# Kernel optimization log

Measured on AMD Instinct MI355X. Metric: run time of the kernel, lower is better.

## Reference

```python
import jax, jax.numpy as jnp
import numpy as np

N_NODES = 50000
N_FEAT = 128
N_EDGES = 1600000
HID = 64


def gcn_conv(x, row, col, w, W, b, n):
    """PyG GCNConv with edge weights and added self-loops (fill_value=1).
    x: [N, Fin]; row/col: [E] (src, dst); w: [E]; W: [Fin, Fout]; b: [Fout].
    """
    loop = jnp.arange(n)
    r = jnp.concatenate([row, loop])
    c = jnp.concatenate([col, loop])
    ww = jnp.concatenate([w, jnp.ones((n,), dtype=x.dtype)])
    deg = jax.ops.segment_sum(ww, c, num_segments=n)  # [N]
    dinv = jnp.where(deg > 0, jax.lax.rsqrt(deg), 0.0)
    norm = dinv[r] * ww * dinv[c]  # [E+N]
    xw = x @ W  # [N, Fout] -- linear before propagate, as in PyG
    msg = norm[:, None] * xw[r]  # gather + scale
    out = jax.ops.segment_sum(msg, c, num_segments=n)  # scatter-add
    return out + b


def setup_inputs() -> dict:
    key = jax.random.key(0)
    ks = jax.random.split(key, 12)
    features = jax.random.normal(ks[0], (N_NODES, N_FEAT), dtype=jnp.float32)
    edge_index = jax.random.randint(ks[1], (2, N_EDGES), 0, N_NODES, dtype=jnp.int64)
    edge_attr = jax.random.uniform(ks[2], (N_EDGES,), dtype=jnp.float32)
    s = 0.05
    # generator encoder: GCNConv(n_feat->64), GCNConv(64->n_feat)
    Wg1 = jax.random.normal(ks[3], (N_FEAT, HID), dtype=jnp.float32) * s
    bg1 = jnp.zeros((HID,), dtype=jnp.float32)
    Wg2 = jax.random.normal(ks[4], (HID, N_FEAT), dtype=jnp.float32) * s
    bg2 = jnp.zeros((N_FEAT,), dtype=jnp.float32)
    # discriminator: GCNConv(n_feat->64), Linear(n_nodes*64 -> 1)
    Wd1 = jax.random.normal(ks[5], (N_FEAT, HID), dtype=jnp.float32) * s
    bd1 = jnp.zeros((HID,), dtype=jnp.float32)
    wfc = jax.random.normal(ks[6], (N_NODES * HID,), dtype=jnp.float32) * 0.001
    bfc = jnp.zeros((), dtype=jnp.float32)
    return {"features": features, "edge_index": edge_index, "edge_attr": edge_attr,
            "Wg1": Wg1, "bg1": bg1, "Wg2": Wg2, "bg2": bg2,
            "Wd1": Wd1, "bd1": bd1, "wfc": wfc, "bfc": bfc}


def reference(features, edge_index, edge_attr, Wg1, bg1, Wg2, bg2, Wd1, bd1, wfc, bfc):
    n = features.shape[0]
    row, col = edge_index[0], edge_index[1]
    # --- generator encoder (eval mode: dropout is a no-op) ---
    h = gcn_conv(features, row, col, edge_attr, Wg1, bg1, n)
    h = jax.nn.relu(h)
    z = jax.nn.sigmoid(gcn_conv(h, row, col, edge_attr, Wg2, bg2, n))  # [N, n_feat]
    # --- GAE inner-product decoder over the given edge list ---
    edge_probs = jax.nn.sigmoid(jnp.sum(z[row] * z[col], axis=-1))  # [E]
    # residual connection
    enc = z + features
    edge_probs = jnp.nan_to_num(edge_probs, nan=0.0)
    # --- discriminator (eval mode: no noise, no dropout) ---
    d = gcn_conv(enc, row, col, edge_probs, Wd1, bd1, n)
    d = jax.nn.relu(d)
    logit = jnp.dot(d.reshape(-1), wfc) + bfc
    return jax.nn.sigmoid(logit)
```

## Files before the change

### kernel.cpp

```cpp
#include <hip/hip_runtime.h>
#include <math.h>

static constexpr int NN = 50000;
static constexpr int NF = 128;
static constexpr int NH = 64;
static constexpr int NE = 1600000;
static constexpr int NBUSED = (NN + 255) / 256;
static constexpr int NWG = 256;
static constexpr int CHUNK = NE / NWG;

typedef unsigned long long u64;


__device__ __forceinline__ float bf2f(unsigned u) { return __uint_as_float(u << 16); }
__device__ __forceinline__ unsigned short f2bf(float f) {
  unsigned b = __float_as_uint(f);
  b += 0x7fffu + ((b >> 16) & 1u);
  return (unsigned short)(b >> 16);
}
__device__ __forceinline__ float sigm(float x) { return 1.f / (1.f + __expf(-x)); }


__global__ __launch_bounds__(256) void bhist_k(const int* __restrict__ col,
                                               int* __restrict__ counts) {
  __shared__ int cnt[256];
  cnt[threadIdx.x] = 0;
  __syncthreads();
  int g = blockIdx.x;
  int e1 = g * CHUNK + CHUNK;
  for (int e = g * CHUNK + threadIdx.x; e < e1; e += 256)
    atomicAdd(&cnt[col[e] >> 8], 1);
  __syncthreads();
  counts[g * 256 + threadIdx.x] = cnt[threadIdx.x];
}

__global__ __launch_bounds__(256) void bscan_k(int* __restrict__ counts) {
  __shared__ int sm[256];
  int b = threadIdx.x;
  int tot = 0;
  for (int g = 0; g < NWG; g++) tot += counts[g * 256 + b];
  sm[b] = tot;
  __syncthreads();
  int v = tot;
  for (int off = 1; off < 256; off <<= 1) {
    int u = (b >= off) ? sm[b - off] : 0;
    __syncthreads();
    sm[b] += u;
    __syncthreads();
  }
  int run = sm[b] - v;
  for (int g = 0; g < NWG; g++) {
    int c = counts[g * 256 + b];
    counts[g * 256 + b] = run;
    run += c;
  }
}

__global__ __launch_bounds__(256) void bpart_k(const int* __restrict__ row,
                                               const int* __restrict__ col,
                                               const float* __restrict__ w,
                                               const int* __restrict__ counts,
                                               u64* __restrict__ ebuf) {
  __shared__ int cur[256];
  int g = blockIdx.x;
  cur[threadIdx.x] = counts[g * 256 + threadIdx.x];
  __syncthreads();
  int e1 = g * CHUNK + CHUNK;
  for (int e = g * CHUNK + threadIdx.x; e < e1; e += 256) {
    int c = col[e];
    int p = atomicAdd(&cur[c >> 8], 1);
    u64 pk = ((u64)(unsigned)__float_as_int(w[e]) << 32) |
             ((unsigned)(c & 255) << 16) | (unsigned)row[e];
    ebuf[p] = pk;
  }
}

__global__ __launch_bounds__(256) void bsortA_k(const u64* __restrict__ ebuf,
                                                const int* __restrict__ counts,
                                                int* __restrict__ rowstart,
                                                float* __restrict__ dinv) {
  __shared__ int cnt[256];
  __shared__ float deg[256];
  __shared__ int sm[256];
  int b = blockIdx.x, t = threadIdx.x;
  cnt[t] = 0;
  deg[t] = 1.0f;
  __syncthreads();
  int boff = counts[b];
  int bend = (b < NBUSED - 1) ? counts[b + 1] : NE;
  for (int e = boff + t; e < bend; e += 256) {
    u64 pk = ebuf[e];
    unsigned lo = (unsigned)pk;
    int c = (lo >> 16) & 255;
    atomicAdd(&cnt[c], 1);
    atomicAdd(&deg[c], __uint_as_float((unsigned)(pk >> 32)));
  }
  __syncthreads();
  int v = cnt[t];
  sm[t] = v;
  __syncthreads();
  for (int off = 1; off < 256; off <<= 1) {
    int u = (t >= off) ? sm[t - off] : 0;
    __syncthreads();
    sm[t] += u;
    __syncthreads();
  }
  int colg = b * 256 + t;
  if (colg < NN) {
    rowstart[colg] = boff + sm[t] - v;
    dinv[colg] = rsqrtf(deg[t]);
  }
  if (b == NBUSED - 1 && t == 0) rowstart[NN] = NE;
}

__global__ __launch_bounds__(256) void bsortB_k(const u64* __restrict__ ebuf,
                                                const int* __restrict__ counts,
                                                const int* __restrict__ rowstart,
                                                const float* __restrict__ dinv,
                                                int2* __restrict__ es) {
  __shared__ int cur[256];
  int b = blockIdx.x, t = threadIdx.x;
  int colg = b * 256 + t;
  cur[t] = (colg < NN) ? rowstart[colg] : NE;
  __syncthreads();
  int boff = counts[b];
  int bend = (b < NBUSED - 1) ? counts[b + 1] : NE;
  for (int e = boff + t; e < bend; e += 256) {
    u64 pk = ebuf[e];
    unsigned lo = (unsigned)pk;
    int r = lo & 0xffff;
    int c = (lo >> 16) & 255;
    float wv = __uint_as_float((unsigned)(pk >> 32));
    int p = atomicAdd(&cur[c], 1);
    es[p] = make_int2(r, __float_as_int(dinv[r] * wv));
  }
}

__global__ void norm2_k(int2* __restrict__ es, const float* __restrict__ ep_s,
                        const float* __restrict__ dinv2, int E) {
  int e = blockIdx.x * 256 + threadIdx.x;
  if (e < E) {
    int2 v = es[e];
    es[e] = make_int2(v.x, __float_as_int(dinv2[v.x] * ep_s[e]));
  }
}

template<int K, int M, int ACT, bool OUTF, bool OUTH, bool XH>
__global__ __launch_bounds__(256) void gemm_k(const float* __restrict__ X,
                                              const unsigned short* __restrict__ Xh,
                                              const float* __restrict__ Xadd,
                                              const float* __restrict__ W,
                                              const float* __restrict__ bias,
                                              float* __restrict__ Yf,
                                              unsigned short* __restrict__ Yh) {
  __shared__ float Ws[K * M];
  __shared__ float Xs[16][K];
  for (int i = threadIdx.x; i < K * M; i += 256) Ws[i] = W[i];
  int r0 = blockIdx.x * 16;
  for (int i = threadIdx.x; i < 16 * K; i += 256) {
    int r = i / K, k = i % K;
    size_t off = (size_t)(r0 + r) * K + k;
    float v = XH ? bf2f(Xh[off]) : X[off];
    if (Xadd) v += Xadd[off];
    Xs[r][k] = v;
  }
  __syncthreads();
  constexpr int RPT = 16 * M / 256;
  constexpr int RS = 256 / M;
  int colc = threadIdx.x % M;
  int rb = threadIdx.x / M;
  float acc[RPT];
#pragma unroll
  for (int i = 0; i < RPT; i++) acc[i] = 0.f;
  for (int k = 0; k < K; k++) {
    float wv = Ws[k * M + colc];
#pragma unroll
    for (int i = 0; i < RPT; i++) acc[i] += Xs[rb + i * RS][k] * wv;
  }
#pragma unroll
  for (int i = 0; i < RPT; i++) {
    int r = r0 + rb + i * RS;
    float o = acc[i];
    if (ACT > 0) o += bias[colc];
    if (ACT == 2) o = sigm(o);
    if (OUTF) Yf[(size_t)r * M + colc] = o;
    if (OUTH) Yh[(size_t)r * M + colc] = f2bf(o);
  }
}

template<int MODE>
__global__ __launch_bounds__(256) void agg64_k(const int* __restrict__ rowstart,
                                               const int2* __restrict__ es,
                                               const unsigned short* __restrict__ src,
                                               const float* __restrict__ dinv,
                                               const float* __restrict__ bias,
                                               unsigned short* __restrict__ outh,
                                               float* __restrict__ outf,
                                               const float* __restrict__ wfc) {
  int wid = (blockIdx.x * 256 + threadIdx.x) >> 6;
  int lane = threadIdx.x & 63;
  int sub = lane >> 4;
  int l = lane & 15;
  int e0 = rowstart[wid], e1 = rowstart[wid + 1];
  float a0 = 0.f, a1 = 0.f, a2 = 0.f, a3 = 0.f;
  for (int eb = e0; eb < e1; eb += 4) {
    int e = eb + sub;
    bool valid = e < e1;
    int2 er = es[valid ? e : eb];
    float nm = valid ? __int_as_float(er.y) : 0.f;
    ushort4 v = *(const ushort4*)(src + (size_t)er.x * 64 + l * 4);
    a0 = fmaf(nm, bf2f(v.x), a0);
    a1 = fmaf(nm, bf2f(v.y), a1);
    a2 = fmaf(nm, bf2f(v.z), a2);
    a3 = fmaf(nm, bf2f(v.w), a3);
  }
  a0 += __shfl_xor(a0, 16); a0 += __shfl_xor(a0, 32);
  a1 += __shfl_xor(a1, 16); a1 += __shfl_xor(a1, 32);
  a2 += __shfl_xor(a2, 16); a2 += __shfl_xor(a2, 32);
  a3 += __shfl_xor(a3, 16); a3 += __shfl_xor(a3, 32);
  float di = dinv[wid];
  ushort4 sv = *(const ushort4*)(src + (size_t)wid * 64 + l * 4);
  float o0 = di * (a0 + di * bf2f(sv.x));
  float o1 = di * (a1 + di * bf2f(sv.y));
  float o2 = di * (a2 + di * bf2f(sv.z));
  float o3 = di * (a3 + di * bf2f(sv.w));
  if (MODE != 1) {
    float4 b = *(const float4*)(bias + l * 4);
    o0 = fmaxf(o0 + b.x, 0.f);
    o1 = fmaxf(o1 + b.y, 0.f);
    o2 = fmaxf(o2 + b.z, 0.f);
    o3 = fmaxf(o3 + b.w, 0.f);
  }
  if (MODE == 0) {
    if (sub == 0) {
      ushort4 p;
      p.x = f2bf(o0); p.y = f2bf(o1); p.z = f2bf(o2); p.w = f2bf(o3);
      *(ushort4*)(outh + (size_t)wid * 64 + l * 4) = p;
    }
  } else if (MODE == 1) {
    if (sub == 0) *(float4*)(outf + (size_t)wid * 64 + l * 4) = make_float4(o0, o1, o2, o3);
  } else {
    float s = 0.f;
    if (sub == 0) {
      float4 w4 = *(const float4*)(wfc + (size_t)wid * 64 + l * 4);
      s = o0 * w4.x + o1 * w4.y + o2 * w4.z + o3 * w4.w;
    }
    s += __shfl_xor(s, 1);
    s += __shfl_xor(s, 2);
    s += __shfl_xor(s, 4);
    s += __shfl_xor(s, 8);
    __shared__ float bs[4];
    if (lane == 0) bs[threadIdx.x >> 6] = s;
    __syncthreads();
    if (threadIdx.x == 0) outf[blockIdx.x] = bs[0] + bs[1] + bs[2] + bs[3];
  }
}

__global__ __launch_bounds__(256) void eprob8_k(const int* __restrict__ rowstart,
                                                const int2* __restrict__ es,
                                                const unsigned short* __restrict__ zh,
                                                float* __restrict__ ep_s,
                                                float* __restrict__ dinv2) {
  int wid = (blockIdx.x * 256 + threadIdx.x) >> 6;
  int lane = threadIdx.x & 63;
  int sub = lane >> 3;
  int l = lane & 7;
  const unsigned short* zp = zh + (size_t)wid * NF + l * 16;
  uint4 zA = *(const uint4*)zp;
  uint4 zB = *(const uint4*)(zp + 8);
  float z0 = bf2f(zA.x & 0xffffu), z1 = bf2f(zA.x >> 16);
  float z2 = bf2f(zA.y & 0xffffu), z3 = bf2f(zA.y >> 16);
  float z4 = bf2f(zA.z & 0xffffu), z5 = bf2f(zA.z >> 16);
  float z6 = bf2f(zA.w & 0xffffu), z7 = bf2f(zA.w >> 16);
  float z8 = bf2f(zB.x & 0xffffu), z9 = bf2f(zB.x >> 16);
  float za = bf2f(zB.y & 0xffffu), zb = bf2f(zB.y >> 16);
  float zc = bf2f(zB.z & 0xffffu), zd = bf2f(zB.z >> 16);
  float ze = bf2f(zB.w & 0xffffu), zf = bf2f(zB.w >> 16);
  int e0 = rowstart[wid], e1 = rowstart[wid + 1];
  float sum = 0.f;
  for (int eb = e0; eb < e1; eb += 8) {
    int e = eb + sub;
    bool valid = e < e1;
    int r = es[valid ? e : eb].x;
    const unsigned short* rp = zh + (size_t)r * NF + l * 16;
    uint4 a = *(const uint4*)rp;
    uint4 b = *(const uint4*)(rp + 8);
    float d;
    d  = bf2f(a.x & 0xffffu) * z0 + bf2f(a.x >> 16) * z1;
    d += bf2f(a.y & 0xffffu) * z2 + bf2f(a.y >> 16) * z3;
    d += bf2f(a.z & 0xffffu) * z4 + bf2f(a.z >> 16) * z5;
    d += bf2f(a.w & 0xffffu) * z6 + bf2f(a.w >> 16) * z7;
    d += bf2f(b.x & 0xffffu) * z8 + bf2f(b.x >> 16) * z9;
    d += bf2f(b.y & 0xffffu) * za + bf2f(b.y >> 16) * zb;
    d += bf2f(b.z & 0xffffu) * zc + bf2f(b.z >> 16) * zd;
    d += bf2f(b.w & 0xffffu) * ze + bf2f(b.w >> 16) * zf;
    d += __shfl_xor(d, 1);
    d += __shfl_xor(d, 2);
    d += __shfl_xor(d, 4);
    if (valid && l == 0) {
      float p = sigm(d);
      ep_s[e] = p;
      sum += p;
    }
  }
  sum += __shfl_xor(sum, 8);
  sum += __shfl_xor(sum, 16);
  sum += __shfl_xor(sum, 32);
  if (lane == 0) dinv2[wid] = rsqrtf(1.f + sum);
}

__global__ __launch_bounds__(256) void reduce_k(const float* __restrict__ partials, int n,
                                                const float* __restrict__ bfc,
                                                float* __restrict__ out) {
  float s = 0.f;
  for (int i = threadIdx.x; i < n; i += 256) s += partials[i];
  s += __shfl_xor(s, 1);
  s += __shfl_xor(s, 2);
  s += __shfl_xor(s, 4);
  s += __shfl_xor(s, 8);
  s += __shfl_xor(s, 16);
  s += __shfl_xor(s, 32);
  __shared__ float ws4[4];
  if ((threadIdx.x & 63) == 0) ws4[threadIdx.x >> 6] = s;
  __syncthreads();
  if (threadIdx.x == 0) out[0] = sigm(ws4[0] + ws4[1] + ws4[2] + ws4[3] + bfc[0]);
}


extern "C" void kernel_launch(void* const* d_in, const int* in_sizes, int n_in,
                              void* d_out, int out_size, void* d_ws, size_t ws_size,
                              hipStream_t stream) {
  const float* features = (const float*)d_in[0];
  const int* edge_index = (const int*)d_in[1];
  const float* edge_attr = (const float*)d_in[2];
  const float* Wg1 = (const float*)d_in[3];
  const float* bg1 = (const float*)d_in[4];
  const float* Wg2 = (const float*)d_in[5];
  const float* bg2 = (const float*)d_in[6];
  const float* Wd1 = (const float*)d_in[7];
  const float* bd1 = (const float*)d_in[8];
  const float* wfc = (const float*)d_in[9];
  const float* bfc = (const float*)d_in[10];
  float* out = (float*)d_out;

  const int* row = edge_index;
  const int* col = edge_index + NE;

  char* wsb = (char*)d_ws;
  auto carve = [&](size_t bytes) {
    void* p = wsb;
    wsb += (bytes + 255) & ~(size_t)255;
    return p;
  };
  int*   counts   = (int*)carve((size_t)NWG * 256 * 4);
  int*   rowstart = (int*)carve((NN + 1) * 4);
  float* dinv     = (float*)carve(NN * 4);
  float* dinv2    = (float*)carve(NN * 4);
  u64*   ebuf     = (u64*)carve((size_t)NE * 8);
  int2*  es       = (int2*)carve((size_t)NE * 8);
  float* ep_s     = (float*)carve((size_t)NE * 4);
  unsigned short* xwh = (unsigned short*)carve((size_t)NN * NH * 2);
  unsigned short* hh  = (unsigned short*)carve((size_t)NN * NH * 2);
  float* ah   = (float*)carve((size_t)NN * NH * 4);
  unsigned short* zh = (unsigned short*)carve((size_t)NN * NF * 2);
  float* partials = (float*)carve(12500 * 4);

  const int GE = (NE + 255) / 256;
  const int GG = NN / 16;
  const int GW = NN * 64 / 256;

  bhist_k<<<NWG, 256, 0, stream>>>(col, counts);
  bscan_k<<<1, 256, 0, stream>>>(counts);
  bpart_k<<<NWG, 256, 0, stream>>>(row, col, edge_attr, counts, ebuf);
  bsortA_k<<<NBUSED, 256, 0, stream>>>(ebuf, counts, rowstart, dinv);
  bsortB_k<<<NBUSED, 256, 0, stream>>>(ebuf, counts, rowstart, dinv, es);

  gemm_k<NF, NH, 0, false, true, false><<<GG, 256, 0, stream>>>(
      features, nullptr, nullptr, Wg1, nullptr, nullptr, xwh);
  agg64_k<0><<<GW, 256, 0, stream>>>(rowstart, es, xwh, dinv, bg1, hh, nullptr, nullptr);

  agg64_k<1><<<GW, 256, 0, stream>>>(rowstart, es, hh, dinv, nullptr, nullptr, ah, nullptr);
  gemm_k<NH, NF, 2, false, true, false><<<GG, 256, 0, stream>>>(
      ah, nullptr, nullptr, Wg2, bg2, nullptr, zh);

  eprob8_k<<<GW, 256, 0, stream>>>(rowstart, es, zh, ep_s, dinv2);

  norm2_k<<<GE, 256, 0, stream>>>(es, ep_s, dinv2, NE);

  gemm_k<NF, NH, 0, false, true, true><<<GG, 256, 0, stream>>>(
      nullptr, zh, features, Wd1, nullptr, nullptr, xwh);
  agg64_k<2><<<GW, 256, 0, stream>>>(rowstart, es, xwh, dinv2, bd1, nullptr, partials, wfc);

  reduce_k<<<1, 256, 0, stream>>>(partials, GW, bfc, out);
}
```

Baseline: 401.0 us.

## Gather FP8 z and discriminator features, fold norm2 into aggregation

Stores z and the discriminator's x@W as FP8 (e4m3 via the hardware cvt builtins) so the edge-probability and final aggregation gathers move half the bytes of the earlier bf16 copies. The separate norm2 pass is removed: eprob writes the edge probability straight into the edge-list slot, and the final aggregation applies dinv2[src] on the fly. The bf16 aggregations now use 16-byte loads with 8 edges per wavefront iteration. The cost is a large drop in precision for z and xw, which risks accuracy tolerance, plus an extra dinv2 gather per edge.

```diff
diff --git a/kernel.cpp b/kernel.cpp
--- a/kernel.cpp
+++ b/kernel.cpp
@@ -10,6 +10,7 @@
 static constexpr int CHUNK = NE / NWG;
 
 typedef unsigned long long u64;
+typedef float f32x2 __attribute__((ext_vector_type(2)));
 
 
 __device__ __forceinline__ float bf2f(unsigned u) { return __uint_as_float(u << 16); }
@@ -19,6 +20,21 @@
   return (unsigned short)(b >> 16);
 }
 __device__ __forceinline__ float sigm(float x) { return 1.f / (1.f + __expf(-x)); }
+__device__ __forceinline__ unsigned char f2fp8(float f) {
+  int v = __builtin_amdgcn_cvt_pk_fp8_f32(f, f, 0, false);
+  return (unsigned char)(v & 0xff);
+}
+__device__ __forceinline__ void fp8x16_dec(uint4 v, float* o) {
+  f32x2 t;
+  t = __builtin_amdgcn_cvt_pk_f32_fp8(v.x, false); o[0] = t.x;  o[1] = t.y;
+  t = __builtin_amdgcn_cvt_pk_f32_fp8(v.x, true);  o[2] = t.x;  o[3] = t.y;
+  t = __builtin_amdgcn_cvt_pk_f32_fp8(v.y, false); o[4] = t.x;  o[5] = t.y;
+  t = __builtin_amdgcn_cvt_pk_f32_fp8(v.y, true);  o[6] = t.x;  o[7] = t.y;
+  t = __builtin_amdgcn_cvt_pk_f32_fp8(v.z, false); o[8] = t.x;  o[9] = t.y;
+  t = __builtin_amdgcn_cvt_pk_f32_fp8(v.z, true);  o[10] = t.x; o[11] = t.y;
+  t = __builtin_amdgcn_cvt_pk_f32_fp8(v.w, false); o[12] = t.x; o[13] = t.y;
+  t = __builtin_amdgcn_cvt_pk_f32_fp8(v.w, true);  o[14] = t.x; o[15] = t.y;
+}
 
 
 __global__ __launch_bounds__(256) void bhist_k(const int* __restrict__ col,
@@ -136,23 +152,15 @@
   }
 }
 
-__global__ void norm2_k(int2* __restrict__ es, const float* __restrict__ ep_s,
-                        const float* __restrict__ dinv2, int E) {
-  int e = blockIdx.x * 256 + threadIdx.x;
-  if (e < E) {
-    int2 v = es[e];
-    es[e] = make_int2(v.x, __float_as_int(dinv2[v.x] * ep_s[e]));
-  }
-}
-
-template<int K, int M, int ACT, bool OUTF, bool OUTH, bool XH>
+template<int K, int M, int ACT, bool OUTF, bool OUTH, bool XH, bool OUT8>
 __global__ __launch_bounds__(256) void gemm_k(const float* __restrict__ X,
                                               const unsigned short* __restrict__ Xh,
                                               const float* __restrict__ Xadd,
                                               const float* __restrict__ W,
                                               const float* __restrict__ bias,
                                               float* __restrict__ Yf,
-                                              unsigned short* __restrict__ Yh) {
+                                              unsigned short* __restrict__ Yh,
+                                              unsigned char* __restrict__ Y8) {
   __shared__ float Ws[K * M];
   __shared__ float Xs[16][K];
   for (int i = threadIdx.x; i < K * M; i += 256) Ws[i] = W[i];
@@ -185,6 +193,7 @@
     if (ACT == 2) o = sigm(o);
     if (OUTF) Yf[(size_t)r * M + colc] = o;
     if (OUTH) Yh[(size_t)r * M + colc] = f2bf(o);
+    if (OUT8) Y8[(size_t)r * M + colc] = f2fp8(o);
   }
 }
 
@@ -192,6 +201,7 @@
 __global__ __launch_bounds__(256) void agg64_k(const int* __restrict__ rowstart,
                                                const int2* __restrict__ es,
                                                const unsigned short* __restrict__ src,
+                                               const unsigned char* __restrict__ src8,
                                                const float* __restrict__ dinv,
                                                const float* __restrict__ bias,
                                                unsigned short* __restrict__ outh,
@@ -199,56 +209,106 @@
                                                const float* __restrict__ wfc) {
   int wid = (blockIdx.x * 256 + threadIdx.x) >> 6;
   int lane = threadIdx.x & 63;
-  int sub = lane >> 4;
-  int l = lane & 15;
   int e0 = rowstart[wid], e1 = rowstart[wid + 1];
-  float a0 = 0.f, a1 = 0.f, a2 = 0.f, a3 = 0.f;
-  for (int eb = e0; eb < e1; eb += 4) {
-    int e = eb + sub;
-    bool valid = e < e1;
-    int2 er = es[valid ? e : eb];
-    float nm = valid ? __int_as_float(er.y) : 0.f;
-    ushort4 v = *(const ushort4*)(src + (size_t)er.x * 64 + l * 4);
-    a0 = fmaf(nm, bf2f(v.x), a0);
-    a1 = fmaf(nm, bf2f(v.y), a1);
-    a2 = fmaf(nm, bf2f(v.z), a2);
-    a3 = fmaf(nm, bf2f(v.w), a3);
-  }
-  a0 += __shfl_xor(a0, 16); a0 += __shfl_xor(a0, 32);
-  a1 += __shfl_xor(a1, 16); a1 += __shfl_xor(a1, 32);
-  a2 += __shfl_xor(a2, 16); a2 += __shfl_xor(a2, 32);
-  a3 += __shfl_xor(a3, 16); a3 += __shfl_xor(a3, 32);
   float di = dinv[wid];
-  ushort4 sv = *(const ushort4*)(src + (size_t)wid * 64 + l * 4);
-  float o0 = di * (a0 + di * bf2f(sv.x));
-  float o1 = di * (a1 + di * bf2f(sv.y));
-  float o2 = di * (a2 + di * bf2f(sv.z));
-  float o3 = di * (a3 + di * bf2f(sv.w));
-  if (MODE != 1) {
-    float4 b = *(const float4*)(bias + l * 4);
-    o0 = fmaxf(o0 + b.x, 0.f);
-    o1 = fmaxf(o1 + b.y, 0.f);
-    o2 = fmaxf(o2 + b.z, 0.f);
-    o3 = fmaxf(o3 + b.w, 0.f);
-  }
-  if (MODE == 0) {
-    if (sub == 0) {
-      ushort4 p;
-      p.x = f2bf(o0); p.y = f2bf(o1); p.z = f2bf(o2); p.w = f2bf(o3);
-      *(ushort4*)(outh + (size_t)wid * 64 + l * 4) = p;
-    }
-  } else if (MODE == 1) {
-    if (sub == 0) *(float4*)(outf + (size_t)wid * 64 + l * 4) = make_float4(o0, o1, o2, o3);
+
+  if (MODE != 2) {
+    int sub = lane >> 3;
+    int l = lane & 7;
+    float a[8];
+#pragma unroll
+    for (int c = 0; c < 8; c++) a[c] = 0.f;
+    for (int eb = e0; eb < e1; eb += 8) {
+      int e = eb + sub;
+      bool valid = e < e1;
+      int2 er = es[valid ? e : eb];
+      float nm = valid ? __int_as_float(er.y) : 0.f;
+      uint4 v = *(const uint4*)(src + (size_t)er.x * 64 + l * 8);
+      a[0] = fmaf(nm, bf2f(v.x & 0xffffu), a[0]);
+      a[1] = fmaf(nm, bf2f(v.x >> 16), a[1]);
+      a[2] = fmaf(nm, bf2f(v.y & 0xffffu), a[2]);
+      a[3] = fmaf(nm, bf2f(v.y >> 16), a[3]);
+      a[4] = fmaf(nm, bf2f(v.z & 0xffffu), a[4]);
+      a[5] = fmaf(nm, bf2f(v.z >> 16), a[5]);
+      a[6] = fmaf(nm, bf2f(v.w & 0xffffu), a[6]);
+      a[7] = fmaf(nm, bf2f(v.w >> 16), a[7]);
+    }
+#pragma unroll
+    for (int c = 0; c < 8; c++) {
+      a[c] += __shfl_xor(a[c], 8);
+      a[c] += __shfl_xor(a[c], 16);
+      a[c] += __shfl_xor(a[c], 32);
+    }
+    uint4 sv = *(const uint4*)(src + (size_t)wid * 64 + l * 8);
+    float sf[8] = {bf2f(sv.x & 0xffffu), bf2f(sv.x >> 16), bf2f(sv.y & 0xffffu),
+                   bf2f(sv.y >> 16),     bf2f(sv.z & 0xffffu), bf2f(sv.z >> 16),
+                   bf2f(sv.w & 0xffffu), bf2f(sv.w >> 16)};
+    float o[8];
+#pragma unroll
+    for (int c = 0; c < 8; c++) o[c] = di * (a[c] + di * sf[c]);
+    if (MODE == 0) {
+      float4 b0 = *(const float4*)(bias + l * 8);
+      float4 b1 = *(const float4*)(bias + l * 8 + 4);
+      o[0] = fmaxf(o[0] + b0.x, 0.f); o[1] = fmaxf(o[1] + b0.y, 0.f);
+      o[2] = fmaxf(o[2] + b0.z, 0.f); o[3] = fmaxf(o[3] + b0.w, 0.f);
+      o[4] = fmaxf(o[4] + b1.x, 0.f); o[5] = fmaxf(o[5] + b1.y, 0.f);
+      o[6] = fmaxf(o[6] + b1.z, 0.f); o[7] = fmaxf(o[7] + b1.w, 0.f);
+      if (sub == 0) {
+        uint4 p;
+        p.x = (unsigned)f2bf(o[0]) | ((unsigned)f2bf(o[1]) << 16);
+        p.y = (unsigned)f2bf(o[2]) | ((unsigned)f2bf(o[3]) << 16);
+        p.z = (unsigned)f2bf(o[4]) | ((unsigned)f2bf(o[5]) << 16);
+        p.w = (unsigned)f2bf(o[6]) | ((unsigned)f2bf(o[7]) << 16);
+        *(uint4*)(outh + (size_t)wid * 64 + l * 8) = p;
+      }
+    } else {
+      if (sub == 0) {
+        *(float4*)(outf + (size_t)wid * 64 + l * 8) = make_float4(o[0], o[1], o[2], o[3]);
+        *(float4*)(outf + (size_t)wid * 64 + l * 8 + 4) = make_float4(o[4], o[5], o[6], o[7]);
+      }
+    }
   } else {
+    int sub = lane >> 2;
+    int l = lane & 3;
+    float a[16];
+#pragma unroll
+    for (int c = 0; c < 16; c++) a[c] = 0.f;
+    for (int eb = e0; eb < e1; eb += 16) {
+      int e = eb + sub;
+      bool valid = e < e1;
+      int2 er = es[valid ? e : eb];
+      float nm = valid ? dinv[er.x] * __int_as_float(er.y) : 0.f;
+      uint4 v = *(const uint4*)(src8 + (size_t)er.x * 64 + l * 16);
+      float t[16];
+      fp8x16_dec(v, t);
+#pragma unroll
+      for (int c = 0; c < 16; c++) a[c] = fmaf(nm, t[c], a[c]);
+    }
+#pragma unroll
+    for (int c = 0; c < 16; c++) {
+      a[c] += __shfl_xor(a[c], 4);
+      a[c] += __shfl_xor(a[c], 8);
+      a[c] += __shfl_xor(a[c], 16);
+      a[c] += __shfl_xor(a[c], 32);
+    }
+    uint4 sv = *(const uint4*)(src8 + (size_t)wid * 64 + l * 16);
+    float sf[16];
+    fp8x16_dec(sv, sf);
     float s = 0.f;
     if (sub == 0) {
-      float4 w4 = *(const float4*)(wfc + (size_t)wid * 64 + l * 4);
-      s = o0 * w4.x + o1 * w4.y + o2 * w4.z + o3 * w4.w;
+#pragma unroll
+      for (int c = 0; c < 4; c++) {
+        float4 b4 = *(const float4*)(bias + l * 16 + c * 4);
+        float4 w4 = *(const float4*)(wfc + (size_t)wid * 64 + l * 16 + c * 4);
+        float o0 = fmaxf(di * (a[c * 4 + 0] + di * sf[c * 4 + 0]) + b4.x, 0.f);
+        float o1 = fmaxf(di * (a[c * 4 + 1] + di * sf[c * 4 + 1]) + b4.y, 0.f);
+        float o2 = fmaxf(di * (a[c * 4 + 2] + di * sf[c * 4 + 2]) + b4.z, 0.f);
+        float o3 = fmaxf(di * (a[c * 4 + 3] + di * sf[c * 4 + 3]) + b4.w, 0.f);
+        s += o0 * w4.x + o1 * w4.y + o2 * w4.z + o3 * w4.w;
+      }
     }
     s += __shfl_xor(s, 1);
     s += __shfl_xor(s, 2);
-    s += __shfl_xor(s, 4);
-    s += __shfl_xor(s, 8);
     __shared__ float bs[4];
     if (lane == 0) bs[threadIdx.x >> 6] = s;
     __syncthreads();
@@ -257,49 +317,34 @@
 }
 
 __global__ __launch_bounds__(256) void eprob8_k(const int* __restrict__ rowstart,
-                                                const int2* __restrict__ es,
-                                                const unsigned short* __restrict__ zh,
-                                                float* __restrict__ ep_s,
+                                                int2* __restrict__ es,
+                                                const unsigned char* __restrict__ z8,
                                                 float* __restrict__ dinv2) {
   int wid = (blockIdx.x * 256 + threadIdx.x) >> 6;
   int lane = threadIdx.x & 63;
   int sub = lane >> 3;
   int l = lane & 7;
-  const unsigned short* zp = zh + (size_t)wid * NF + l * 16;
-  uint4 zA = *(const uint4*)zp;
-  uint4 zB = *(const uint4*)(zp + 8);
-  float z0 = bf2f(zA.x & 0xffffu), z1 = bf2f(zA.x >> 16);
-  float z2 = bf2f(zA.y & 0xffffu), z3 = bf2f(zA.y >> 16);
-  float z4 = bf2f(zA.z & 0xffffu), z5 = bf2f(zA.z >> 16);
-  float z6 = bf2f(zA.w & 0xffffu), z7 = bf2f(zA.w >> 16);
-  float z8 = bf2f(zB.x & 0xffffu), z9 = bf2f(zB.x >> 16);
-  float za = bf2f(zB.y & 0xffffu), zb = bf2f(zB.y >> 16);
-  float zc = bf2f(zB.z & 0xffffu), zd = bf2f(zB.z >> 16);
-  float ze = bf2f(zB.w & 0xffffu), zf = bf2f(zB.w >> 16);
+  uint4 zv = *(const uint4*)(z8 + (size_t)wid * NF + l * 16);
+  float zi[16];
+  fp8x16_dec(zv, zi);
   int e0 = rowstart[wid], e1 = rowstart[wid + 1];
   float sum = 0.f;
   for (int eb = e0; eb < e1; eb += 8) {
     int e = eb + sub;
     bool valid = e < e1;
     int r = es[valid ? e : eb].x;
-    const unsigned short* rp = zh + (size_t)r * NF + l * 16;
-    uint4 a = *(const uint4*)rp;
-    uint4 b = *(const uint4*)(rp + 8);
-    float d;
-    d  = bf2f(a.x & 0xffffu) * z0 + bf2f(a.x >> 16) * z1;
-    d += bf2f(a.y & 0xffffu) * z2 + bf2f(a.y >> 16) * z3;
-    d += bf2f(a.z & 0xffffu) * z4 + bf2f(a.z >> 16) * z5;
-    d += bf2f(a.w & 0xffffu) * z6 + bf2f(a.w >> 16) * z7;
-    d += bf2f(b.x & 0xffffu) * z8 + bf2f(b.x >> 16) * z9;
-    d += bf2f(b.y & 0xffffu) * za + bf2f(b.y >> 16) * zb;
-    d += bf2f(b.z & 0xffffu) * zc + bf2f(b.z >> 16) * zd;
-    d += bf2f(b.w & 0xffffu) * ze + bf2f(b.w >> 16) * zf;
+    uint4 v = *(const uint4*)(z8 + (size_t)r * NF + l * 16);
+    float zr[16];
+    fp8x16_dec(v, zr);
+    float d = 0.f;
+#pragma unroll
+    for (int c = 0; c < 16; c++) d = fmaf(zr[c], zi[c], d);
     d += __shfl_xor(d, 1);
     d += __shfl_xor(d, 2);
     d += __shfl_xor(d, 4);
     if (valid && l == 0) {
       float p = sigm(d);
-      ep_s[e] = p;
+      es[e].y = __float_as_int(p);
       sum += p;
     }
   }
@@ -358,14 +403,14 @@
   float* dinv2    = (float*)carve(NN * 4);
   u64*   ebuf     = (u64*)carve((size_t)NE * 8);
   int2*  es       = (int2*)carve((size_t)NE * 8);
-  float* ep_s     = (float*)carve((size_t)NE * 4);
   unsigned short* xwh = (unsigned short*)carve((size_t)NN * NH * 2);
   unsigned short* hh  = (unsigned short*)carve((size_t)NN * NH * 2);
   float* ah   = (float*)carve((size_t)NN * NH * 4);
   unsigned short* zh = (unsigned short*)carve((size_t)NN * NF * 2);
+  unsigned char* z8  = (unsigned char*)carve((size_t)NN * NF);
+  unsigned char* xw8 = (unsigned char*)carve((size_t)NN * NH);
   float* partials = (float*)carve(12500 * 4);
 
-  const int GE = (NE + 255) / 256;
   const int GG = NN / 16;
   const int GW = NN * 64 / 256;
 
@@ -375,21 +420,22 @@
   bsortA_k<<<NBUSED, 256, 0, stream>>>(ebuf, counts, rowstart, dinv);
   bsortB_k<<<NBUSED, 256, 0, stream>>>(ebuf, counts, rowstart, dinv, es);
 
-  gemm_k<NF, NH, 0, false, true, false><<<GG, 256, 0, stream>>>(
-      features, nullptr, nullptr, Wg1, nullptr, nullptr, xwh);
-  agg64_k<0><<<GW, 256, 0, stream>>>(rowstart, es, xwh, dinv, bg1, hh, nullptr, nullptr);
-
-  agg64_k<1><<<GW, 256, 0, stream>>>(rowstart, es, hh, dinv, nullptr, nullptr, ah, nullptr);
-  gemm_k<NH, NF, 2, false, true, false><<<GG, 256, 0, stream>>>(
-      ah, nullptr, nullptr, Wg2, bg2, nullptr, zh);
-
-  eprob8_k<<<GW, 256, 0, stream>>>(rowstart, es, zh, ep_s, dinv2);
-
-  norm2_k<<<GE, 256, 0, stream>>>(es, ep_s, dinv2, NE);
-
-  gemm_k<NF, NH, 0, false, true, true><<<GG, 256, 0, stream>>>(
-      nullptr, zh, features, Wd1, nullptr, nullptr, xwh);
-  agg64_k<2><<<GW, 256, 0, stream>>>(rowstart, es, xwh, dinv2, bd1, nullptr, partials, wfc);
+  gemm_k<NF, NH, 0, false, true, false, false><<<GG, 256, 0, stream>>>(
+      features, nullptr, nullptr, Wg1, nullptr, nullptr, xwh, nullptr);
+  agg64_k<0><<<GW, 256, 0, stream>>>(rowstart, es, xwh, nullptr, dinv, bg1, hh, nullptr,
+                                     nullptr);
+
+  agg64_k<1><<<GW, 256, 0, stream>>>(rowstart, es, hh, nullptr, dinv, nullptr, nullptr, ah,
+                                     nullptr);
+  gemm_k<NH, NF, 2, false, true, false, true><<<GG, 256, 0, stream>>>(
+      ah, nullptr, nullptr, Wg2, bg2, nullptr, zh, z8);
+
+  eprob8_k<<<GW, 256, 0, stream>>>(rowstart, es, z8, dinv2);
+
+  gemm_k<NF, NH, 0, false, false, true, true><<<GG, 256, 0, stream>>>(
+      nullptr, zh, features, Wd1, nullptr, nullptr, nullptr, xw8);
+  agg64_k<2><<<GW, 256, 0, stream>>>(rowstart, es, nullptr, xw8, dinv2, bd1, nullptr,
+                                     partials, wfc);
 
   reduce_k<<<1, 256, 0, stream>>>(partials, GW, bfc, out);
 }
```

Measured after the change: 341.2 us. -14.9%, faster.
